# Kernel optimization log

Hardware: AMD Instinct MI355X
Metric: run time of the kernel (lower is better)

## Reference

```python
import jax, jax.numpy as jnp
import numpy as np

KS = 32        # kernel_size (chunk size)
STRIDE = 16    # kernel_stride
H = 8          # head_num_k
D = 128        # head_dim
B = 4          # number of sequences
SEQ = 8192     # tokens per sequence (equal-length varlen batch)


def setup_inputs() -> dict:
    key = jax.random.key(0)
    k1, k2, k3, k4, k5 = jax.random.split(key, 5)
    kv = jax.random.normal(k1, (B * SEQ, 2, H, D), dtype=jnp.float32)
    cu_seqlens = jnp.arange(B + 1, dtype=jnp.int32) * SEQ
    # torch Conv1d default init: uniform(-s, s), s = 1/sqrt(in_channels*kernel_size)
    s = 1.0 / np.sqrt(D * KS)
    k_conv_w = jax.random.uniform(k2, (D, D, KS), jnp.float32, -s, s)
    k_conv_b = jax.random.uniform(k3, (D,), jnp.float32, -s, s)
    v_conv_w = jax.random.uniform(k4, (D, D, KS), jnp.float32, -s, s)
    v_conv_b = jax.random.uniform(k5, (D,), jnp.float32, -s, s)
    return {"kv": kv, "cu_seqlens": cu_seqlens,
            "k_conv_w": k_conv_w, "k_conv_b": k_conv_b,
            "v_conv_w": v_conv_w, "v_conv_b": v_conv_b}


def _chunk_indices(cu_seqlens, total_tokens):
    # Equal-length sequences: every strided chunk is valid, so shapes are static.
    batch = cu_seqlens.shape[0] - 1
    seqlen = total_tokens // batch
    nc = (seqlen - KS) // STRIDE + 1  # chunks per sequence
    starts = cu_seqlens[:-1].astype(jnp.int32)          # [B]
    offs = (jnp.arange(nc, dtype=jnp.int32) * STRIDE)   # [nc]
    pos = jnp.arange(KS, dtype=jnp.int32)               # [KS]
    idx = starts[:, None, None] + offs[None, :, None] + pos[None, None, :]  # [B, nc, KS]
    cu_comp = jnp.arange(batch + 1, dtype=jnp.int32) * nc
    return idx.reshape(batch * nc, KS), cu_comp


def reference(kv, cu_seqlens, k_conv_w, k_conv_b, v_conv_w, v_conv_b):
    idx, cu_comp = _chunk_indices(cu_seqlens, kv.shape[0])  # [L, KS]
    filtered = kv[idx.reshape(-1)].reshape(idx.shape[0], KS, 2, H, D)  # [L, KS, 2, H, D]
    k = filtered[:, :, 0]  # [L, KS, H, D]
    v = filtered[:, :, 1]
    # Conv1d with kernel spanning the whole chunk -> single output position:
    # out[l,h,o] = sum_{i,t} x[l,t,h,i] * W[o,i,t] + b[o]
    compress_k = jnp.einsum('lthi,oit->lho', k, k_conv_w) + k_conv_b
    compress_v = jnp.einsum('lthi,oit->lho', v, v_conv_w) + v_conv_b
    return compress_k, compress_v, cu_comp
```

## Files before the change

kernel.cpp:

```cpp
#include <hip/hip_runtime.h>

typedef __attribute__((ext_vector_type(8))) short bf16x8;
typedef __attribute__((ext_vector_type(4))) float f32x4;

#define MFMA16(A, B, C) __builtin_amdgcn_mfma_f32_16x16x32_bf16(A, B, C, 0, 0, 0)

__device__ __forceinline__ unsigned short f2bf(float f) {
  union { float f; unsigned int u; } v; v.f = f;
  return (unsigned short)((v.u + 0x7fffu + ((v.u >> 16) & 1u)) >> 16);
}
#define PK(LO, HI) (((unsigned int)f2bf(LO)) | ((unsigned int)f2bf(HI) << 16))

#define BAR() do {                                              \
    asm volatile("s_waitcnt lgkmcnt(0)" ::: "memory");          \
    __builtin_amdgcn_s_barrier();                               \
    asm volatile("" ::: "memory");                              \
  } while (0)

__global__ __launch_bounds__(256) void prep_kernel(
    const float* __restrict__ kw, const float* __restrict__ vw,
    unsigned short* __restrict__ imgK, unsigned short* __restrict__ imgV,
    int KSd,
    const int* __restrict__ cuin, float* __restrict__ outf,
    int cubase, int nb, int strideh) {
  __shared__ float wlds[4096];
  int tid = threadIdx.x, bid = blockIdx.x;
  int sel = bid >> 7, o = bid & 127;
  int nel = 128 * KSd;
  const float* wo = (sel ? vw : kw) + (size_t)o * nel;
  unsigned short* dst = sel ? imgV : imgK;
  for (int i = tid; i < (nel >> 2); i += 256)
    ((float4*)wlds)[i] = ((const float4*)wo)[i];
  __syncthreads();
  int swE = (o & 7) << 3;
  for (int idx = tid; idx < nel; idx += 256) {
    int s = idx >> 6, c = idx & 63;
    int i = ((s & 1) << 6) + (c ^ swE);
    dst[((size_t)s << 13) + (o << 6) + c] = f2bf(wlds[i * KSd + (s >> 1)]);
  }
  if (bid == 0 && tid <= nb) outf[cubase + tid] = (float)(cuin[tid] / strideh);
}

__global__ __launch_bounds__(512) void gemm_big_kernel(
    const float* __restrict__ kv,
    const float* __restrict__ biasK, const float* __restrict__ biasV,
    const unsigned short* __restrict__ imgK, const unsigned short* __restrict__ imgV,
    float* __restrict__ out,
    int vbase, int nc, int ltot, int tokmax, int seqb, int mtiles) {
  __shared__ __align__(16) unsigned short T[2][16640];
  __shared__ __align__(16) unsigned short Bs[2][8192];
  int tid = threadIdx.x, bid = blockIdx.x;
  int per_sel = 8 * mtiles;
  int sel = (bid >= per_sel) ? 1 : 0;
  int rem = bid - sel * per_sel;
  int h = rem / mtiles, mtile = rem - h * mtiles;
  int m0 = mtile * 128;
  const unsigned short* img = sel ? imgV : imgK;
  const float* bias = sel ? biasV : biasK;
  int outbase = sel ? vbase : 0;
  int lane = tid & 63, wid = tid >> 6;
  int wm = wid >> 2, wn = wid & 3;
  int l15 = lane & 15, l4 = lane >> 4;

  int b0 = m0 / nc, c0 = m0 - b0 * nc;
  int btok0 = b0 * seqb + c0 * 16;
  int rb = nc - c0;

  int sjl = tid >> 4, sje = tid & 15;
  int soff = sel * 1024 + h * 128 + sje * 8;

  int kb0 = l4 * 16;
  int jbL[4], jswL[4], jbH[4], jswH[4];
#pragma unroll
  for (int mi = 0; mi < 4; ++mi) {
    int r = wm * 64 + mi * 16 + l15;
    int j = r + (r >= rb ? 1 : 0);
    jbL[mi] = j * 256;       jswL[mi] = (j & 7) << 4;
    jbH[mi] = (j + 1) * 256; jswH[mi] = ((j + 1) & 7) << 4;
  }

  int o0 = wn * 32 + l15, o1 = o0 + 16;
  int brb0 = o0 * 128, bsw0 = (o0 & 7) << 4;
  int brb1 = o1 * 128, bsw1 = (o1 & 7) << 4;

  f32x4 zz = {0.f, 0.f, 0.f, 0.f};
  f32x4 acc[4][2];
#pragma unroll
  for (int mi = 0; mi < 4; ++mi) { acc[mi][0] = zz; acc[mi][1] = zz; }

  float4 ta[5], tb[5];
  uint4 BrA0, BrA1, BrB0, BrB1;

#define STAGE_LOAD(P) do {                                                       \
    _Pragma("unroll")                                                            \
    for (int q_ = 0; q_ < 4; ++q_) {                                             \
      int t_ = btok0 + (q_ * 32 + sjl) * 16 + (P); if (t_ > tokmax) t_ = tokmax; \
      const float* a_ = kv + ((size_t)t_ << 11) + soff;                          \
      ta[q_] = *(const float4*)a_; tb[q_] = *(const float4*)(a_ + 4);            \
    }                                                                            \
    if (sjl < 2) {                                                               \
      int t_ = btok0 + (128 + sjl) * 16 + (P); if (t_ > tokmax) t_ = tokmax;     \
      const float* a_ = kv + ((size_t)t_ << 11) + soff;                          \
      ta[4] = *(const float4*)a_; tb[4] = *(const float4*)(a_ + 4);              \
    }                                                                            \
  } while (0)

#define T_WRITE(TB) do {                                                         \
    char* tp_ = (char*)(TB);                                                     \
    _Pragma("unroll")                                                            \
    for (int q_ = 0; q_ < 4; ++q_) {                                             \
      int js_ = q_ * 32 + sjl;                                                   \
      *(uint4*)(tp_ + js_ * 256 + ((sje * 16) ^ ((js_ & 7) << 4))) =             \
        make_uint4(PK(ta[q_].x, ta[q_].y), PK(ta[q_].z, ta[q_].w),               \
                   PK(tb[q_].x, tb[q_].y), PK(tb[q_].z, tb[q_].w));              \
    }                                                                            \
    if (sjl < 2) {                                                               \
      int js_ = 128 + sjl;                                                       \
      *(uint4*)(tp_ + js_ * 256 + ((sje * 16) ^ ((js_ & 7) << 4))) =             \
        make_uint4(PK(ta[4].x, ta[4].y), PK(ta[4].z, ta[4].w),                   \
                   PK(tb[4].x, tb[4].y), PK(tb[4].z, tb[4].w));                  \
    }                                                                            \
  } while (0)

#define B_LOAD(R0, R1, S) do {                                                   \
    const uint4* bsrc_ = (const uint4*)(img + ((size_t)(S) << 13));              \
    R0 = bsrc_[tid];                                                             \
    R1 = bsrc_[512 + tid];                                                       \
  } while (0)

#define B_WRITE(DB, R0, R1) do {                                                 \
    uint4* bdst_ = (uint4*)Bs[DB];                                               \
    bdst_[tid] = R0;                                                             \
    bdst_[512 + tid] = R1;                                                       \
  } while (0)

#define SUBSTEP(HF, JB, JSW, BB) do {                                            \
    const char* tc_ = (const char*)T[tcur];                                      \
    const char* bc_ = (const char*)Bs[BB];                                       \
    __builtin_amdgcn_s_setprio(1);                                               \
    _Pragma("unroll")                                                            \
    for (int kk = 0; kk < 2; ++kk) {                                             \
      int kcA_ = (HF) * 128 + kk * 64 + kb0;                                     \
      int kcB_ = kk * 64 + kb0;                                                  \
      bf16x8 b0_ = *(const bf16x8*)(bc_ + brb0 + (kcB_ ^ bsw0));                 \
      bf16x8 b1_ = *(const bf16x8*)(bc_ + brb1 + (kcB_ ^ bsw1));                 \
      _Pragma("unroll")                                                          \
      for (int mi = 0; mi < 4; ++mi) {                                           \
        bf16x8 a_ = *(const bf16x8*)(tc_ + JB[mi] + (kcA_ ^ JSW[mi]));           \
        acc[mi][0] = MFMA16(a_, b0_, acc[mi][0]);                                \
        acc[mi][1] = MFMA16(a_, b1_, acc[mi][1]);                                \
      }                                                                          \
    }                                                                            \
    __builtin_amdgcn_s_setprio(0);                                               \
  } while (0)

  int tcur = 0;
  STAGE_LOAD(0);
  T_WRITE(T[0]);
  B_LOAD(BrA0, BrA1, 0);
  B_WRITE(0, BrA0, BrA1);
  B_LOAD(BrB0, BrB1, 1);
  B_LOAD(BrA0, BrA1, 32);
  BAR();

  for (int p = 0; p < 16; ++p) {
    if (p < 15) STAGE_LOAD(p + 1);
    SUBSTEP(0, jbL, jswL, 0);
    B_WRITE(1, BrB0, BrB1);
    B_LOAD(BrB0, BrB1, 2 * p + 33);
    BAR();
    SUBSTEP(1, jbL, jswL, 1);
    B_WRITE(0, BrA0, BrA1);
    if (p < 15) B_LOAD(BrA0, BrA1, 2 * p + 2);
    BAR();
    SUBSTEP(0, jbH, jswH, 0);
    B_WRITE(1, BrB0, BrB1);
    if (p < 15) B_LOAD(BrB0, BrB1, 2 * p + 3);
    BAR();
    SUBSTEP(1, jbH, jswH, 1);
    if (p < 15) {
      B_WRITE(0, BrA0, BrA1);
      B_LOAD(BrA0, BrA1, 2 * p + 34);
      T_WRITE(T[tcur ^ 1]);
      BAR();
    }
    tcur ^= 1;
  }

#pragma unroll
  for (int ni = 0; ni < 2; ++ni) {
    int o_ = wn * 32 + ni * 16 + l15;
    float bv_ = bias[o_];
#pragma unroll
    for (int mi = 0; mi < 4; ++mi) {
      int lb_ = m0 + wm * 64 + mi * 16 + l4 * 4;
      f32x4 v_ = acc[mi][ni];
#pragma unroll
      for (int jj = 0; jj < 4; ++jj) {
        int ll_ = lb_ + jj;
        if (ll_ < ltot)
          out[(size_t)outbase + (size_t)ll_ * 1024 + h * 128 + o_] = v_[jj] + bv_;
      }
    }
  }
}

__global__ __launch_bounds__(512) void gemm_kernel(
    const float* __restrict__ kv,
    const float* __restrict__ biasK, const float* __restrict__ biasV,
    const unsigned short* __restrict__ imgK, const unsigned short* __restrict__ imgV,
    const float* __restrict__ kw, const float* __restrict__ vw,
    float* __restrict__ out,
    int selbase, int vbase, int nc, int ltot, int nsteps,
    int tokmax, int seqb, int strideh, int KSd, int mtiles) {
  __shared__ __align__(16) unsigned short As[2][4096];
  __shared__ __align__(16) unsigned short Bsf[2][8192];
  int tid = threadIdx.x, bid = blockIdx.x;
  int per_sel = 8 * mtiles;
  int sel = selbase + (bid >= per_sel);
  int rem = (bid >= per_sel) ? bid - per_sel : bid;
  int h = rem / mtiles, mtile = rem - h * mtiles;
  int m0 = mtile * 64;
  const unsigned short* img = sel ? imgV : imgK;
  const float* bias = sel ? biasV : biasK;
  const float* wsel = sel ? vw : kw;
  int outbase = sel ? vbase : 0;
  int lane = tid & 63, wid = tid >> 6;
  int warpM = wid >> 2, warpN = wid & 3;

  int aj = tid & 7, r = tid >> 3;
  int l = m0 + r; if (l > ltot - 1) l = ltot - 1;
  int b = l / nc, c = l - b * nc;
  int btok = b * seqb + c * strideh;
  const float* abase = kv + sel * 1024 + h * 128 + aj * 4;
  int swr = (r & 7) << 3;
  int awb0 = r * 128 + 2 * ((aj * 4) ^ swr);
  int awb1 = r * 128 + 2 * ((aj * 4 + 32) ^ swr);

  int o_g = tid >> 3, cb_g = (tid & 7) << 3;
  int ib_g = cb_g ^ ((o_g & 7) << 3);
  const float* g0 = wsel + (size_t)o_g * (KSd << 7);
  const float* g1 = g0 + ((size_t)64 * (KSd << 7));

  int kb0 = (lane >> 4) * 16;
  int arb[2], asw[2], brb[2], bsw[2];
#pragma unroll
  for (int mi = 0; mi < 2; ++mi) {
    int rr = warpM * 32 + mi * 16 + (lane & 15);
    arb[mi] = rr * 128; asw[mi] = (rr & 7) << 4;
  }
#pragma unroll
  for (int ni = 0; ni < 2; ++ni) {
    int oo = warpN * 32 + ni * 16 + (lane & 15);
    brb[ni] = oo * 128; bsw[ni] = (oo & 7) << 4;
  }

  f32x4 acc[2][2];
  f32x4 zz = {0.f, 0.f, 0.f, 0.f};
#pragma unroll
  for (int a = 0; a < 2; ++a)
#pragma unroll
    for (int b2 = 0; b2 < 2; ++b2) acc[a][b2] = zz;

  float4 Af0, Af1;
  uint4 Brr[2];

#define LOAD_STEP(S) do {                                                        \
    int tok_ = btok + ((S) >> 1); if (tok_ > tokmax) tok_ = tokmax;              \
    const float* ap_ = abase + ((size_t)tok_ << 11) + (((S) & 1) << 6);          \
    Af0 = *(const float4*)ap_;                                                   \
    Af1 = *(const float4*)(ap_ + 32);                                            \
    if (img) {                                                                   \
      const uint4* bsrc_ = (const uint4*)(img + ((size_t)(S) << 13));            \
      Brr[0] = bsrc_[tid];                                                       \
      Brr[1] = bsrc_[512 + tid];                                                 \
    } else {                                                                     \
      int t_ = (S) >> 1, i0_ = (((S) & 1) << 6) + ib_g;                          \
      unsigned int p0_[4], p1_[4];                                               \
      _Pragma("unroll")                                                          \
      for (int m = 0; m < 4; ++m) {                                              \
        p0_[m] = (unsigned int)f2bf(g0[(i0_ + 2*m) * KSd + t_])                  \
               | ((unsigned int)f2bf(g0[(i0_ + 2*m + 1) * KSd + t_]) << 16);     \
        p1_[m] = (unsigned int)f2bf(g1[(i0_ + 2*m) * KSd + t_])                  \
               | ((unsigned int)f2bf(g1[(i0_ + 2*m + 1) * KSd + t_]) << 16);     \
      }                                                                          \
      Brr[0] = make_uint4(p0_[0], p0_[1], p0_[2], p0_[3]);                       \
      Brr[1] = make_uint4(p1_[0], p1_[1], p1_[2], p1_[3]);                       \
    }                                                                            \
  } while (0)

#define WRITE_STEP(DB) do {                                                      \
    *(uint2*)((char*)As[DB] + awb0) = make_uint2(PK(Af0.x, Af0.y), PK(Af0.z, Af0.w)); \
    *(uint2*)((char*)As[DB] + awb1) = make_uint2(PK(Af1.x, Af1.y), PK(Af1.z, Af1.w)); \
    uint4* bdst_ = (uint4*)Bsf[DB];                                              \
    bdst_[tid] = Brr[0];                                                         \
    bdst_[512 + tid] = Brr[1];                                                   \
  } while (0)

#define COMPUTE_STEP(CB) do {                                                    \
    _Pragma("unroll")                                                            \
    for (int kk = 0; kk < 2; ++kk) {                                             \
      bf16x8 af_[2], bg_[2];                                                     \
      int kc_ = kk * 64 + kb0;                                                   \
      _Pragma("unroll")                                                          \
      for (int mi = 0; mi < 2; ++mi)                                             \
        af_[mi] = *(const bf16x8*)((const char*)As[CB] + arb[mi] + (kc_ ^ asw[mi])); \
      _Pragma("unroll")                                                          \
      for (int ni = 0; ni < 2; ++ni)                                             \
        bg_[ni] = *(const bf16x8*)((const char*)Bsf[CB] + brb[ni] + (kc_ ^ bsw[ni])); \
      _Pragma("unroll")                                                          \
      for (int mi = 0; mi < 2; ++mi)                                             \
      _Pragma("unroll")                                                          \
        for (int ni = 0; ni < 2; ++ni)                                           \
          acc[mi][ni] = MFMA16(af_[mi], bg_[ni], acc[mi][ni]);                   \
    }                                                                            \
  } while (0)

  LOAD_STEP(0);
  WRITE_STEP(0);
  __syncthreads();
  int cur = 0;
  for (int s = 0; s < nsteps; ++s) {
    if (s + 1 < nsteps) LOAD_STEP(s + 1);
    COMPUTE_STEP(cur);
    if (s + 1 < nsteps) WRITE_STEP(cur ^ 1);
    __syncthreads();
    cur ^= 1;
  }

  int l15 = lane & 15, l4 = lane >> 4;
#pragma unroll
  for (int ni = 0; ni < 2; ++ni) {
    int o = warpN * 32 + ni * 16 + l15;
    float bv = bias[o];
#pragma unroll
    for (int mi = 0; mi < 2; ++mi) {
      int lb = m0 + warpM * 32 + mi * 16 + l4 * 4;
      f32x4 v = acc[mi][ni];
#pragma unroll
      for (int jj = 0; jj < 4; ++jj) {
        int ll = lb + jj;
        if (ll < ltot)
          out[(size_t)outbase + (size_t)ll * 1024 + h * 128 + o] = v[jj] + bv;
      }
    }
  }
}

extern "C" void kernel_launch(void* const* d_in, const int* in_sizes, int n_in,
                              void* d_out, int out_size, void* d_ws, size_t ws_size,
                              hipStream_t stream) {
  long kvN = 0; int kvi = 0;
  for (int i = 0; i < n_in; ++i)
    if ((long)in_sizes[i] > kvN) { kvN = in_sizes[i]; kvi = i; }
  const float* kv = (const float*)d_in[kvi];
  const float *w0 = nullptr, *w1 = nullptr, *b0 = nullptr, *b1 = nullptr;
  const int* cuin = nullptr;
  int KSd = 32, nb = 4;
  for (int i = 0; i < n_in; ++i) {
    if (i == kvi) continue;
    int sz = in_sizes[i];
    if (sz == 128) { if (!b0) b0 = (const float*)d_in[i]; else if (!b1) b1 = (const float*)d_in[i]; }
    else if (sz <= 32) { nb = sz - 1; cuin = (const int*)d_in[i]; }
    else if (sz >= 4096) {
      if (!w0) { w0 = (const float*)d_in[i]; KSd = sz / 16384; }
      else if (!w1) w1 = (const float*)d_in[i];
    }
  }
  if (!w0) w0 = (const float*)d_in[2];
  if (!b0) b0 = (const float*)d_in[3];
  if (!w1) w1 = (const float*)d_in[4];
  if (!b1) b1 = (const float*)d_in[5];
  if (!cuin) cuin = (const int*)d_in[1];
  if (nb < 1) nb = 4;

  float* out = (float*)d_out;

  int cubase  = out_size - (nb + 1);
  int vbase   = cubase >> 1;
  int ltot    = cubase >> 11;
  int nc      = ltot / nb;
  int nsteps  = 2 * KSd;
  long tokens = kvN >> 11;
  int seqb    = (int)(tokens / nb);
  int strideh = (nc > 1) ? (seqb - KSd) / (nc - 1) : KSd;
  int tokmax  = (int)tokens - 1;
  int mtiles  = (ltot + 63) >> 6;
  int mt128   = (ltot + 127) >> 7;
  int per_sel = 8 * mtiles;

  size_t imgel = (size_t)nsteps * 8192;
  size_t imgbytes = imgel * 2;
  bool fast = (KSd == 32) && (strideh == 16) && (nc >= 128) &&
              (ws_size >= 2 * imgbytes);
  if (fast) {
    unsigned short* imgK = (unsigned short*)d_ws;
    unsigned short* imgV = imgK + imgel;
    prep_kernel<<<256, 256, 0, stream>>>(w0, w1, imgK, imgV, KSd,
                                         cuin, out, cubase, nb, strideh);
    gemm_big_kernel<<<2 * 8 * mt128, 512, 0, stream>>>(
        kv, b0, b1, imgK, imgV, out, vbase, nc, ltot, tokmax, seqb, mt128);
  } else if (ws_size >= 2 * imgbytes) {
    unsigned short* imgK = (unsigned short*)d_ws;
    unsigned short* imgV = imgK + imgel;
    prep_kernel<<<256, 256, 0, stream>>>(w0, w1, imgK, imgV, KSd,
                                         cuin, out, cubase, nb, strideh);
    gemm_kernel<<<2 * per_sel, 512, 0, stream>>>(kv, b0, b1, imgK, imgV, w0, w1, out,
        0, vbase, nc, ltot, nsteps, tokmax, seqb, strideh, KSd, mtiles);
  } else {
    prep_kernel<<<256, 256, 0, stream>>>(w0, w1, (unsigned short*)d_ws,
                                         (unsigned short*)d_ws, 0,
                                         cuin, out, cubase, nb, strideh);
    gemm_kernel<<<2 * per_sel, 512, 0, stream>>>(kv, b0, b1,
        (const unsigned short*)nullptr, (const unsigned short*)nullptr, w0, w1, out,
        0, vbase, nc, ltot, nsteps, tokmax, seqb, strideh, KSd, mtiles);
  }
}
```

Measured before the change: 77.44 us.

## Load weight fragments directly into registers instead of staging through LDS

The GEMM kernel no longer copies each weight step into a double-buffered shared-memory tile. Each lane now reads its own MFMA B fragments straight from the global (L2-resident) bf16 image into registers, with a one-step register prefetch. This removes the LDS write traffic for B and three of the four barriers per iteration. It also frees 32 KB of LDS, at the cost of redundant global reads across waves and more live registers. Separately, the prep kernel pads its shared-memory transpose to avoid bank conflicts.

```diff
diff --git a/kernel.cpp b/kernel.cpp
--- a/kernel.cpp
+++ b/kernel.cpp
@@ -23,32 +23,35 @@
     int KSd,
     const int* __restrict__ cuin, float* __restrict__ outf,
     int cubase, int nb, int strideh) {
-  __shared__ float wlds[4096];
+  __shared__ float wlds[128 * 33];
   int tid = threadIdx.x, bid = blockIdx.x;
   int sel = bid >> 7, o = bid & 127;
   int nel = 128 * KSd;
+  int ksh = (KSd == 32) ? 5 : ((KSd == 16) ? 4 : 31 - __clz(KSd));
+  int pad = KSd + 1;
   const float* wo = (sel ? vw : kw) + (size_t)o * nel;
   unsigned short* dst = sel ? imgV : imgK;
-  for (int i = tid; i < (nel >> 2); i += 256)
-    ((float4*)wlds)[i] = ((const float4*)wo)[i];
+  for (int idx = tid; idx < nel; idx += 256) {
+    int i = idx >> ksh, t = idx & (KSd - 1);
+    wlds[i * pad + t] = wo[idx];
+  }
   __syncthreads();
   int swE = (o & 7) << 3;
   for (int idx = tid; idx < nel; idx += 256) {
     int s = idx >> 6, c = idx & 63;
     int i = ((s & 1) << 6) + (c ^ swE);
-    dst[((size_t)s << 13) + (o << 6) + c] = f2bf(wlds[i * KSd + (s >> 1)]);
+    dst[((size_t)s << 13) + (o << 6) + c] = f2bf(wlds[i * pad + (s >> 1)]);
   }
   if (bid == 0 && tid <= nb) outf[cubase + tid] = (float)(cuin[tid] / strideh);
 }
 
-__global__ __launch_bounds__(512) void gemm_big_kernel(
+__global__ __launch_bounds__(512) void gemm_breg2_kernel(
     const float* __restrict__ kv,
     const float* __restrict__ biasK, const float* __restrict__ biasV,
     const unsigned short* __restrict__ imgK, const unsigned short* __restrict__ imgV,
     float* __restrict__ out,
     int vbase, int nc, int ltot, int tokmax, int seqb, int mtiles) {
   __shared__ __align__(16) unsigned short T[2][16640];
-  __shared__ __align__(16) unsigned short Bs[2][8192];
   int tid = threadIdx.x, bid = blockIdx.x;
   int per_sel = 8 * mtiles;
   int sel = (bid >= per_sel) ? 1 : 0;
@@ -80,8 +83,12 @@
   }
 
   int o0 = wn * 32 + l15, o1 = o0 + 16;
-  int brb0 = o0 * 128, bsw0 = (o0 & 7) << 4;
-  int brb1 = o1 * 128, bsw1 = (o1 & 7) << 4;
+  int swE0 = (o0 & 7) << 3, swE1 = (o1 & 7) << 3;
+  int ke = l4 * 8;
+  int bo00 = o0 * 64 + ((ke) ^ swE0);
+  int bo01 = o1 * 64 + ((ke) ^ swE1);
+  int bo10 = o0 * 64 + ((32 + ke) ^ swE0);
+  int bo11 = o1 * 64 + ((32 + ke) ^ swE1);
 
   f32x4 zz = {0.f, 0.f, 0.f, 0.f};
   f32x4 acc[4][2];
@@ -89,7 +96,7 @@
   for (int mi = 0; mi < 4; ++mi) { acc[mi][0] = zz; acc[mi][1] = zz; }
 
   float4 ta[5], tb[5];
-  uint4 BrA0, BrA1, BrB0, BrB1;
+  bf16x8 Bc0, Bc1, Bc2, Bc3, Bn0, Bn1, Bn2, Bn3;
 
 #define STAGE_LOAD(P) do {                                                       \
     _Pragma("unroll")                                                            \
@@ -122,33 +129,39 @@
     }                                                                            \
   } while (0)
 
-#define B_LOAD(R0, R1, S) do {                                                   \
-    const uint4* bsrc_ = (const uint4*)(img + ((size_t)(S) << 13));              \
-    R0 = bsrc_[tid];                                                             \
-    R1 = bsrc_[512 + tid];                                                       \
-  } while (0)
-
-#define B_WRITE(DB, R0, R1) do {                                                 \
-    uint4* bdst_ = (uint4*)Bs[DB];                                               \
-    bdst_[tid] = R0;                                                             \
-    bdst_[512 + tid] = R1;                                                       \
-  } while (0)
-
-#define SUBSTEP(HF, JB, JSW, BB) do {                                            \
+#define B_LOADR(D0, D1, D2, D3, S) do {                                          \
+    const unsigned short* bp_ = img + ((size_t)(S) << 13);                       \
+    D0 = *(const bf16x8*)(bp_ + bo00);                                           \
+    D1 = *(const bf16x8*)(bp_ + bo01);                                           \
+    D2 = *(const bf16x8*)(bp_ + bo10);                                           \
+    D3 = *(const bf16x8*)(bp_ + bo11);                                           \
+  } while (0)
+
+#define SUBSTEP(HF, JB, JSW, B00, B01, B10, B11) do {                            \
     const char* tc_ = (const char*)T[tcur];                                      \
-    const char* bc_ = (const char*)Bs[BB];                                       \
     __builtin_amdgcn_s_setprio(1);                                               \
-    _Pragma("unroll")                                                            \
-    for (int kk = 0; kk < 2; ++kk) {                                             \
-      int kcA_ = (HF) * 128 + kk * 64 + kb0;                                     \
-      int kcB_ = kk * 64 + kb0;                                                  \
-      bf16x8 b0_ = *(const bf16x8*)(bc_ + brb0 + (kcB_ ^ bsw0));                 \
-      bf16x8 b1_ = *(const bf16x8*)(bc_ + brb1 + (kcB_ ^ bsw1));                 \
+    {                                                                            \
+      int kcA_ = (HF) * 128 + kb0;                                               \
+      bf16x8 a_[4];                                                              \
+      _Pragma("unroll")                                                          \
+      for (int mi = 0; mi < 4; ++mi)                                             \
+        a_[mi] = *(const bf16x8*)(tc_ + JB[mi] + (kcA_ ^ JSW[mi]));              \
       _Pragma("unroll")                                                          \
       for (int mi = 0; mi < 4; ++mi) {                                           \
-        bf16x8 a_ = *(const bf16x8*)(tc_ + JB[mi] + (kcA_ ^ JSW[mi]));           \
-        acc[mi][0] = MFMA16(a_, b0_, acc[mi][0]);                                \
-        acc[mi][1] = MFMA16(a_, b1_, acc[mi][1]);                                \
+        acc[mi][0] = MFMA16(a_[mi], B00, acc[mi][0]);                            \
+        acc[mi][1] = MFMA16(a_[mi], B01, acc[mi][1]);                            \
+      }                                                                          \
+    }                                                                            \
+    {                                                                            \
+      int kcA_ = (HF) * 128 + 64 + kb0;                                          \
+      bf16x8 a_[4];                                                              \
+      _Pragma("unroll")                                                          \
+      for (int mi = 0; mi < 4; ++mi)                                             \
+        a_[mi] = *(const bf16x8*)(tc_ + JB[mi] + (kcA_ ^ JSW[mi]));              \
+      _Pragma("unroll")                                                          \
+      for (int mi = 0; mi < 4; ++mi) {                                           \
+        acc[mi][0] = MFMA16(a_[mi], B10, acc[mi][0]);                            \
+        acc[mi][1] = MFMA16(a_[mi], B11, acc[mi][1]);                            \
       }                                                                          \
     }                                                                            \
     __builtin_amdgcn_s_setprio(0);                                               \
@@ -157,30 +170,21 @@
   int tcur = 0;
   STAGE_LOAD(0);
   T_WRITE(T[0]);
-  B_LOAD(BrA0, BrA1, 0);
-  B_WRITE(0, BrA0, BrA1);
-  B_LOAD(BrB0, BrB1, 1);
-  B_LOAD(BrA0, BrA1, 32);
+  B_LOADR(Bc0, Bc1, Bc2, Bc3, 0);
+  B_LOADR(Bn0, Bn1, Bn2, Bn3, 1);
   BAR();
 
   for (int p = 0; p < 16; ++p) {
     if (p < 15) STAGE_LOAD(p + 1);
-    SUBSTEP(0, jbL, jswL, 0);
-    B_WRITE(1, BrB0, BrB1);
-    B_LOAD(BrB0, BrB1, 2 * p + 33);
-    BAR();
-    SUBSTEP(1, jbL, jswL, 1);
-    B_WRITE(0, BrA0, BrA1);
-    if (p < 15) B_LOAD(BrA0, BrA1, 2 * p + 2);
-    BAR();
-    SUBSTEP(0, jbH, jswH, 0);
-    B_WRITE(1, BrB0, BrB1);
-    if (p < 15) B_LOAD(BrB0, BrB1, 2 * p + 3);
-    BAR();
-    SUBSTEP(1, jbH, jswH, 1);
+    SUBSTEP(0, jbL, jswL, Bc0, Bc1, Bc2, Bc3);
+    B_LOADR(Bc0, Bc1, Bc2, Bc3, 2 * p + 32);
+    SUBSTEP(1, jbL, jswL, Bn0, Bn1, Bn2, Bn3);
+    B_LOADR(Bn0, Bn1, Bn2, Bn3, 2 * p + 33);
+    SUBSTEP(0, jbH, jswH, Bc0, Bc1, Bc2, Bc3);
+    if (p < 15) B_LOADR(Bc0, Bc1, Bc2, Bc3, 2 * p + 2);
+    SUBSTEP(1, jbH, jswH, Bn0, Bn1, Bn2, Bn3);
     if (p < 15) {
-      B_WRITE(0, BrA0, BrA1);
-      B_LOAD(BrA0, BrA1, 2 * p + 34);
+      B_LOADR(Bn0, Bn1, Bn2, Bn3, 2 * p + 3);
       T_WRITE(T[tcur ^ 1]);
       BAR();
     }
@@ -398,7 +402,7 @@
     unsigned short* imgV = imgK + imgel;
     prep_kernel<<<256, 256, 0, stream>>>(w0, w1, imgK, imgV, KSd,
                                          cuin, out, cubase, nb, strideh);
-    gemm_big_kernel<<<2 * 8 * mt128, 512, 0, stream>>>(
+    gemm_breg2_kernel<<<2 * 8 * mt128, 512, 0, stream>>>(
         kv, b0, b1, imgK, imgV, out, vbase, nc, ltot, tokmax, seqb, mt128);
   } else if (ws_size >= 2 * imgbytes) {
     unsigned short* imgK = (unsigned short*)d_ws;
```

After: 79.64 us. 2.8% more time.
